# Kernel tuning notes

Measured on AMD Instinct MI355X. Metric: run time of the kernel, lower is better.

## Reference

```python
import jax, jax.numpy as jnp
import numpy as np

N = 50000
E = 800000
IN_C = 128
MSG_C = 64
OUT_C = 128


def setup_inputs() -> dict:
    key = jax.random.key(0)
    ks = jax.random.split(key, 10)
    x = jax.random.normal(ks[0], (N, IN_C), dtype=jnp.float32)
    edge_index = jax.random.randint(ks[1], (2, E), 0, N, dtype=jnp.int64)
    message = jax.random.normal(ks[2], (E, MSG_C), dtype=jnp.float32)
    # MLP params (Linear stores [out,in] in torch; we keep [in,out] for x @ W)
    s1 = 1.0 / np.sqrt(IN_C + MSG_C)
    s2 = 1.0 / np.sqrt(OUT_C)
    W1 = jax.random.uniform(ks[3], (IN_C + MSG_C, OUT_C), minval=-s1, maxval=s1, dtype=jnp.float32)
    b1 = jax.random.uniform(ks[4], (OUT_C,), minval=-s1, maxval=s1, dtype=jnp.float32)
    W2 = jax.random.uniform(ks[5], (OUT_C, OUT_C), minval=-s2, maxval=s2, dtype=jnp.float32)
    b2 = jax.random.uniform(ks[6], (OUT_C,), minval=-s2, maxval=s2, dtype=jnp.float32)
    W3 = jax.random.uniform(ks[7], (OUT_C, OUT_C), minval=-s2, maxval=s2, dtype=jnp.float32)
    gamma = jnp.ones((OUT_C,), dtype=jnp.float32)
    beta = jnp.zeros((OUT_C,), dtype=jnp.float32)
    return {"x": x, "edge_index": edge_index, "message": message,
            "W1": W1, "b1": b1, "W2": W2, "b2": b2, "W3": W3,
            "gamma": gamma, "beta": beta}


def _layer_norm(h, gamma, beta, eps=1e-5):
    mu = jnp.mean(h, axis=-1, keepdims=True)
    var = jnp.mean((h - mu) ** 2, axis=-1, keepdims=True)
    return (h - mu) * jax.lax.rsqrt(var + eps) * gamma + beta


def reference(x, edge_index, message, W1, b1, W2, b2, W3, gamma, beta):
    dest = edge_index[1]
    # scatter-add messages into N node slots: [E, msg] -> [N, msg]
    msg_aggr = jax.ops.segment_sum(message, dest, num_segments=N)
    h = jnp.concatenate([x, msg_aggr], axis=-1)  # [N, in+msg]
    h = jax.nn.leaky_relu(h @ W1 + b1, negative_slope=0.2)
    h = jax.nn.leaky_relu(h @ W2 + b2, negative_slope=0.2)
    h = h @ W3  # no bias
    return _layer_norm(h, gamma, beta)
```

## Files before the change

kernel.cpp:

```cpp
#include <hip/hip_runtime.h>

#define N_NODES 50000
#define N_EDGES 800000
#define IN_C 128
#define MSG_C 64
#define OUT_C 128
#define SCAN_NB 49

typedef __attribute__((ext_vector_type(8))) short short8v;
typedef __attribute__((ext_vector_type(4))) float f32x4;
typedef __attribute__((ext_vector_type(2))) unsigned int u32x2;
typedef __attribute__((ext_vector_type(4))) unsigned int u32x4;

__device__ __forceinline__ unsigned short f2bf(float f) {
    union { float f; unsigned int u; } v; v.f = f;
    unsigned int r = (v.u + 0x7FFFu + ((v.u >> 16) & 1u)) >> 16;
    return (unsigned short)r;
}
__device__ __forceinline__ float bflo(unsigned u) {
    union { unsigned u; float f; } v; v.u = u << 16; return v.f;
}
__device__ __forceinline__ float bfhi(unsigned u) {
    union { unsigned u; float f; } v; v.u = u & 0xFFFF0000u; return v.f;
}

__global__ __launch_bounds__(256) void init_kernel(
    int4* __restrict__ deg4,
    const float* __restrict__ W1, const float* __restrict__ W2,
    const float* __restrict__ W3, unsigned short* __restrict__ Wt1,
    unsigned short* __restrict__ Wt2, unsigned short* __restrict__ Wt3)
{
    int idx = blockIdx.x * 256 + threadIdx.x;
    if (idx < 12500) deg4[idx] = make_int4(0, 0, 0, 0);
    if (idx < 24576) {
        int k = idx >> 7, n = idx & 127;
        Wt1[n * 192 + k] = f2bf(W1[idx]);
    } else if (idx < 40960) {
        int t = idx - 24576;
        int k = t >> 7, n = t & 127;
        Wt2[n * 128 + k] = f2bf(W2[t]);
    } else if (idx < 57344) {
        int t = idx - 40960;
        int k = t >> 7, n = t & 127;
        Wt3[n * 128 + k] = f2bf(W3[t]);
    }
}

__global__ __launch_bounds__(256) void hist_kernel(const int* __restrict__ edge_index,
                                                   int* __restrict__ deg)
{
    int i = blockIdx.x * 256 + threadIdx.x;
    if (i >= N_EDGES / 4) return;
    int4 d4 = *reinterpret_cast<const int4*>(edge_index + N_EDGES + i * 4);
    atomicAdd(&deg[d4.x], 1);
    atomicAdd(&deg[d4.y], 1);
    atomicAdd(&deg[d4.z], 1);
    atomicAdd(&deg[d4.w], 1);
}

__global__ __launch_bounds__(1024) void scan_a_kernel(const int* __restrict__ deg,
                                                      int* __restrict__ offsets,
                                                      int* __restrict__ bsum)
{
    __shared__ int wsum[16];
    const int tid = threadIdx.x, lane = tid & 63, wid = tid >> 6;
    int i = blockIdx.x * 1024 + tid;
    int v = (i < N_NODES) ? deg[i] : 0;
    int s = v;
    #pragma unroll
    for (int d = 1; d < 64; d <<= 1) {
        int t = __shfl_up(s, d);
        if (lane >= d) s += t;
    }
    if (lane == 63) wsum[wid] = s;
    __syncthreads();
    if (wid == 0 && lane < 16) {
        int ws = wsum[lane];
        int ss = ws;
        #pragma unroll
        for (int d = 1; d < 16; d <<= 1) {
            int t = __shfl_up(ss, d);
            if (lane >= d) ss += t;
        }
        wsum[lane] = ss - ws;
    }
    __syncthreads();
    if (i < N_NODES) offsets[i] = s - v + wsum[wid];
    if (tid == 1023) bsum[blockIdx.x] = wsum[15] + s;
}

__global__ __launch_bounds__(1024) void scan_bc_kernel(int* __restrict__ offsets,
                                                       int* __restrict__ cursor,
                                                       const int* __restrict__ bsum)
{
    __shared__ int bpre_s, btot_s;
    const int tid = threadIdx.x;
    if (tid < 64) {
        int v = (tid < SCAN_NB) ? bsum[tid] : 0;
        int s = v;
        #pragma unroll
        for (int d = 1; d < 64; d <<= 1) {
            int t = __shfl_up(s, d);
            if (tid >= d) s += t;
        }
        if (tid == (int)blockIdx.x) bpre_s = s - v;
        if (tid == SCAN_NB - 1) btot_s = s;
    }
    __syncthreads();
    int i = blockIdx.x * 1024 + tid;
    if (i < N_NODES) {
        int o = offsets[i] + bpre_s;
        offsets[i] = o;
        cursor[i] = o;
    }
    if (blockIdx.x == 0 && tid == 0) offsets[N_NODES] = btot_s;
}

__global__ __launch_bounds__(256) void permute_kernel(
    const int* __restrict__ edge_index, const float* __restrict__ message,
    int* __restrict__ cursor, unsigned int* __restrict__ pbuf)
{
    int t = blockIdx.x * 256 + threadIdx.x;
    int e = t >> 4;
    if (e >= N_EDGES) return;
    int lane = threadIdx.x & 63;
    int s = lane & 15;
    int dest = edge_index[N_EDGES + e];
    int pos = 0;
    if (s == 0) pos = atomicAdd(&cursor[dest], 1);
    pos = __shfl(pos, lane & 48);
    f32x4 v = __builtin_nontemporal_load(
        reinterpret_cast<const f32x4*>(message + (long)e * MSG_C + s * 4));
    u32x2 p;
    p.x = (unsigned)f2bf(v.x) | ((unsigned)f2bf(v.y) << 16);
    p.y = (unsigned)f2bf(v.z) | ((unsigned)f2bf(v.w) << 16);
    __builtin_nontemporal_store(p,
        reinterpret_cast<u32x2*>(pbuf + (long)pos * 32 + s * 2));
}

__global__ __launch_bounds__(256) void segsum_kernel(const int* __restrict__ offsets,
                                                     const u32x4* __restrict__ pbuf4,
                                                     unsigned int* __restrict__ aggr_u32)
{
    const int wid = threadIdx.x >> 6;
    const int lane = threadIdx.x & 63;
    int n = blockIdx.x * 4 + wid;
    if (n >= N_NODES) return;
    int s0 = offsets[n], e0 = offsets[n + 1];
    long base = (long)s0 * 8;
    int cnt = (e0 - s0) * 8;
    float a0 = 0.f, a1 = 0.f, a2 = 0.f, a3 = 0.f,
          a4 = 0.f, a5 = 0.f, a6 = 0.f, a7 = 0.f;
    for (int k = lane; k < cnt; k += 64) {
        u32x4 u = __builtin_nontemporal_load(pbuf4 + base + k);
        a0 += bflo(u.x); a1 += bfhi(u.x);
        a2 += bflo(u.y); a3 += bfhi(u.y);
        a4 += bflo(u.z); a5 += bfhi(u.z);
        a6 += bflo(u.w); a7 += bfhi(u.w);
    }
    #pragma unroll
    for (int m = 8; m <= 32; m <<= 1) {
        a0 += __shfl_xor(a0, m); a1 += __shfl_xor(a1, m);
        a2 += __shfl_xor(a2, m); a3 += __shfl_xor(a3, m);
        a4 += __shfl_xor(a4, m); a5 += __shfl_xor(a5, m);
        a6 += __shfl_xor(a6, m); a7 += __shfl_xor(a7, m);
    }
    if (lane < 8) {
        u32x4 p;
        p.x = (unsigned)f2bf(a0) | ((unsigned)f2bf(a1) << 16);
        p.y = (unsigned)f2bf(a2) | ((unsigned)f2bf(a3) << 16);
        p.z = (unsigned)f2bf(a4) | ((unsigned)f2bf(a5) << 16);
        p.w = (unsigned)f2bf(a6) | ((unsigned)f2bf(a7) << 16);
        *reinterpret_cast<u32x4*>(aggr_u32 + (long)n * 32 + lane * 4) = p;
    }
}

__device__ __forceinline__ void stage_load(const unsigned short* __restrict__ Wt,
                                           int KW, int k0, int tid, u32x4 r[4])
{
    const u32x4* src = reinterpret_cast<const u32x4*>(
        Wt + (size_t)(tid >> 1) * KW + k0 + (tid & 1) * 32);
    r[0] = src[0]; r[1] = src[1]; r[2] = src[2]; r[3] = src[3];
}

__device__ __forceinline__ void stage_write(unsigned short* __restrict__ sw,
                                            int tid, const u32x4 r[4])
{
    u32x4* dst = reinterpret_cast<u32x4*>(sw + (tid >> 1) * 72 + (tid & 1) * 32);
    dst[0] = r[0]; dst[1] = r[1]; dst[2] = r[2]; dst[3] = r[3];
}

template<int KW, bool BIAS>
__device__ __forceinline__ void gemm_layer_lds(
    const unsigned short* __restrict__ Wt, const float* __restrict__ bias,
    unsigned short* __restrict__ sW,
    const short8v* af, int tid, int lr, int lg, f32x4 acc[8])
{
    constexpr int NCH = KW / 64;
    #pragma unroll
    for (int ct = 0; ct < 8; ++ct) {
        float bv = BIAS ? bias[ct * 16 + lr] : 0.f;
        acc[ct] = (f32x4){bv, bv, bv, bv};
    }
    u32x4 r[4];
    stage_load(Wt, KW, 0, tid, r);
    stage_write(sW, tid, r);
    __syncthreads();
    #pragma unroll
    for (int c = 0; c < NCH; ++c) {
        if (c + 1 < NCH) stage_load(Wt, KW, (c + 1) * 64, tid, r);
        const unsigned short* swc = sW + (c & 1) * (128 * 72);
        #pragma unroll
        for (int k2 = 0; k2 < 2; ++k2) {
            #pragma unroll
            for (int ct = 0; ct < 8; ++ct) {
                short8v b = *reinterpret_cast<const short8v*>(
                    swc + (ct * 16 + lr) * 72 + k2 * 32 + lg * 8);
                acc[ct] = __builtin_amdgcn_mfma_f32_16x16x32_bf16(
                    af[c * 2 + k2], b, acc[ct], 0, 0, 0);
            }
        }
        if (c + 1 < NCH) stage_write(sW + ((c + 1) & 1) * (128 * 72), tid, r);
        __syncthreads();
    }
}

__device__ __forceinline__ void store_h_leaky(unsigned short* __restrict__ H,
                                              int lr, int lg, const f32x4 acc[8])
{
    #pragma unroll
    for (int ct = 0; ct < 8; ++ct)
        #pragma unroll
        for (int j = 0; j < 4; ++j) {
            float v = acc[ct][j];
            v = v > 0.f ? v : 0.2f * v;
            H[(lg * 4 + j) * 136 + ct * 16 + lr] = f2bf(v);
        }
}

__global__ __launch_bounds__(256, 2) void mlp_mfma_kernel(
    const float* __restrict__ x, const unsigned short* __restrict__ aggr_bf,
    const unsigned short* __restrict__ Wt1, const float* __restrict__ b1,
    const unsigned short* __restrict__ Wt2, const float* __restrict__ b2,
    const unsigned short* __restrict__ Wt3, const float* __restrict__ gamma,
    const float* __restrict__ beta, float* __restrict__ out)
{
    __shared__ __align__(16) unsigned short sA0[4][16][200];
    __shared__ __align__(16) unsigned short sH[4][16][136];
    __shared__ __align__(16) unsigned short sW[2 * 128 * 72];

    const int tid = threadIdx.x;
    const int w = tid >> 6, l = tid & 63;
    const int lr = l & 15, lg = l >> 4;
    const int R0 = blockIdx.x * 64 + w * 16;
    const bool act = (R0 < N_NODES);

    #pragma unroll
    for (int i = 0; i < 4; ++i) {
        int r = lg + i * 4;
        int c0 = lr * 8;
        int gr = R0 + r;
        float4 v0 = {}, v1 = {};
        if (gr < N_NODES) {
            const float4* xp = reinterpret_cast<const float4*>(x + (size_t)gr * IN_C + c0);
            v0 = xp[0]; v1 = xp[1];
        }
        uint4 p;
        p.x = (unsigned)f2bf(v0.x) | ((unsigned)f2bf(v0.y) << 16);
        p.y = (unsigned)f2bf(v0.z) | ((unsigned)f2bf(v0.w) << 16);
        p.z = (unsigned)f2bf(v1.x) | ((unsigned)f2bf(v1.y) << 16);
        p.w = (unsigned)f2bf(v1.z) | ((unsigned)f2bf(v1.w) << 16);
        *reinterpret_cast<uint4*>(&sA0[w][r][c0]) = p;
    }
    #pragma unroll
    for (int i = 0; i < 2; ++i) {
        int r = (l >> 3) + i * 8;
        int c0 = (l & 7) * 8;
        int gr = R0 + r;
        uint4 a4 = {};
        if (gr < N_NODES)
            a4 = *reinterpret_cast<const uint4*>(aggr_bf + (size_t)gr * MSG_C + c0);
        *reinterpret_cast<uint4*>(&sA0[w][r][IN_C + c0]) = a4;
    }

    f32x4 acc[8];
    short8v af[6];

    #pragma unroll
    for (int ks = 0; ks < 6; ++ks)
        af[ks] = *reinterpret_cast<const short8v*>(&sA0[w][lr][ks * 32 + lg * 8]);
    gemm_layer_lds<192, true>(Wt1, b1, sW, af, tid, lr, lg, acc);
    store_h_leaky(&sH[w][0][0], lr, lg, acc);

    #pragma unroll
    for (int ks = 0; ks < 4; ++ks)
        af[ks] = *reinterpret_cast<const short8v*>(&sH[w][lr][ks * 32 + lg * 8]);
    gemm_layer_lds<128, true>(Wt2, b2, sW, af, tid, lr, lg, acc);
    store_h_leaky(&sH[w][0][0], lr, lg, acc);

    #pragma unroll
    for (int ks = 0; ks < 4; ++ks)
        af[ks] = *reinterpret_cast<const short8v*>(&sH[w][lr][ks * 32 + lg * 8]);
    gemm_layer_lds<128, false>(Wt3, nullptr, sW, af, tid, lr, lg, acc);

    float g8[8], be8[8];
    #pragma unroll
    for (int ct = 0; ct < 8; ++ct) {
        g8[ct] = gamma[ct * 16 + lr];
        be8[ct] = beta[ct * 16 + lr];
    }
    #pragma unroll
    for (int j = 0; j < 4; ++j) {
        float s1 = 0.f, s2 = 0.f;
        #pragma unroll
        for (int ct = 0; ct < 8; ++ct) {
            float v = acc[ct][j];
            s1 += v; s2 += v * v;
        }
        #pragma unroll
        for (int m = 8; m >= 1; m >>= 1) {
            s1 += __shfl_xor(s1, m);
            s2 += __shfl_xor(s2, m);
        }
        float mu = s1 * (1.f / 128.f);
        float var = s2 * (1.f / 128.f) - mu * mu;
        float rs = rsqrtf(var + 1e-5f);
        int gr = R0 + lg * 4 + j;
        if (act && gr < N_NODES) {
            #pragma unroll
            for (int ct = 0; ct < 8; ++ct)
                out[(size_t)gr * OUT_C + ct * 16 + lr] =
                    (acc[ct][j] - mu) * rs * g8[ct] + be8[ct];
        }
    }
}

extern "C" void kernel_launch(void* const* d_in, const int* in_sizes, int n_in,
                              void* d_out, int out_size, void* d_ws, size_t ws_size,
                              hipStream_t stream)
{
    const float* x       = (const float*)d_in[0];
    const int*   edge    = (const int*)d_in[1];
    const float* message = (const float*)d_in[2];
    const float* W1      = (const float*)d_in[3];
    const float* b1      = (const float*)d_in[4];
    const float* W2      = (const float*)d_in[5];
    const float* b2      = (const float*)d_in[6];
    const float* W3      = (const float*)d_in[7];
    const float* gamma   = (const float*)d_in[8];
    const float* beta    = (const float*)d_in[9];
    float* out  = (float*)d_out;

    char* ws = (char*)d_ws;
    unsigned short* aggr_bf = (unsigned short*)(ws);
    int*   deg     = (int*)(ws + 6400000);
    int*   cursor  = (int*)(ws + 6600000);
    int*   offsets = (int*)(ws + 6800000);
    int*   bsum    = (int*)(ws + 7000016);
    unsigned short* Wt1 = (unsigned short*)(ws + 7000224);
    unsigned short* Wt2 = (unsigned short*)(ws + 7049376);
    unsigned short* Wt3 = (unsigned short*)(ws + 7082144);
    unsigned int* pbuf  = (unsigned int*)(ws + 7115008);

    init_kernel<<<224, 256, 0, stream>>>((int4*)deg, W1, W2, W3, Wt1, Wt2, Wt3);

    int qblocks = (N_EDGES / 4 + 255) / 256;
    hist_kernel<<<qblocks, 256, 0, stream>>>(edge, deg);
    scan_a_kernel<<<SCAN_NB, 1024, 0, stream>>>(deg, offsets, bsum);
    scan_bc_kernel<<<SCAN_NB, 1024, 0, stream>>>(offsets, cursor, bsum);

    permute_kernel<<<N_EDGES * 16 / 256, 256, 0, stream>>>(edge, message, cursor, pbuf);

    segsum_kernel<<<(N_NODES + 3) / 4, 256, 0, stream>>>(
        offsets, (const u32x4*)pbuf, (unsigned int*)aggr_bf);

    mlp_mfma_kernel<<<(N_NODES + 63) / 64, 256, 0, stream>>>(
        x, aggr_bf, Wt1, b1, Wt2, b2, Wt3, gamma, beta, out);
}
```

Before: 165.5 us.

## Fuse segment-sum aggregation into MLP kernel prologue

Removes the separate segsum kernel. Each wavefront in the MLP kernel now reduces the permuted bf16 messages for its 16 rows and writes the sums straight into shared memory. This drops one launch and the write and re-read of the aggregated buffer in global memory. The cost is that the reduction loop runs serially per row within a wave, with less parallelism and latency hiding than the standalone kernel, which could stall the MFMA stage.

```diff
diff --git a/kernel.cpp b/kernel.cpp
--- a/kernel.cpp
+++ b/kernel.cpp
@@ -138,43 +138,6 @@
         reinterpret_cast<u32x2*>(pbuf + (long)pos * 32 + s * 2));
 }
 
-__global__ __launch_bounds__(256) void segsum_kernel(const int* __restrict__ offsets,
-                                                     const u32x4* __restrict__ pbuf4,
-                                                     unsigned int* __restrict__ aggr_u32)
-{
-    const int wid = threadIdx.x >> 6;
-    const int lane = threadIdx.x & 63;
-    int n = blockIdx.x * 4 + wid;
-    if (n >= N_NODES) return;
-    int s0 = offsets[n], e0 = offsets[n + 1];
-    long base = (long)s0 * 8;
-    int cnt = (e0 - s0) * 8;
-    float a0 = 0.f, a1 = 0.f, a2 = 0.f, a3 = 0.f,
-          a4 = 0.f, a5 = 0.f, a6 = 0.f, a7 = 0.f;
-    for (int k = lane; k < cnt; k += 64) {
-        u32x4 u = __builtin_nontemporal_load(pbuf4 + base + k);
-        a0 += bflo(u.x); a1 += bfhi(u.x);
-        a2 += bflo(u.y); a3 += bfhi(u.y);
-        a4 += bflo(u.z); a5 += bfhi(u.z);
-        a6 += bflo(u.w); a7 += bfhi(u.w);
-    }
-    #pragma unroll
-    for (int m = 8; m <= 32; m <<= 1) {
-        a0 += __shfl_xor(a0, m); a1 += __shfl_xor(a1, m);
-        a2 += __shfl_xor(a2, m); a3 += __shfl_xor(a3, m);
-        a4 += __shfl_xor(a4, m); a5 += __shfl_xor(a5, m);
-        a6 += __shfl_xor(a6, m); a7 += __shfl_xor(a7, m);
-    }
-    if (lane < 8) {
-        u32x4 p;
-        p.x = (unsigned)f2bf(a0) | ((unsigned)f2bf(a1) << 16);
-        p.y = (unsigned)f2bf(a2) | ((unsigned)f2bf(a3) << 16);
-        p.z = (unsigned)f2bf(a4) | ((unsigned)f2bf(a5) << 16);
-        p.w = (unsigned)f2bf(a6) | ((unsigned)f2bf(a7) << 16);
-        *reinterpret_cast<u32x4*>(aggr_u32 + (long)n * 32 + lane * 4) = p;
-    }
-}
-
 __device__ __forceinline__ void stage_load(const unsigned short* __restrict__ Wt,
                                            int KW, int k0, int tid, u32x4 r[4])
 {
@@ -239,7 +202,8 @@
 }
 
 __global__ __launch_bounds__(256, 2) void mlp_mfma_kernel(
-    const float* __restrict__ x, const unsigned short* __restrict__ aggr_bf,
+    const float* __restrict__ x, const int* __restrict__ offsets,
+    const u32x4* __restrict__ pbuf4,
     const unsigned short* __restrict__ Wt1, const float* __restrict__ b1,
     const unsigned short* __restrict__ Wt2, const float* __restrict__ b2,
     const unsigned short* __restrict__ Wt3, const float* __restrict__ gamma,
@@ -272,15 +236,44 @@
         p.w = (unsigned)f2bf(v1.z) | ((unsigned)f2bf(v1.w) << 16);
         *reinterpret_cast<uint4*>(&sA0[w][r][c0]) = p;
     }
-    #pragma unroll
-    for (int i = 0; i < 2; ++i) {
-        int r = (l >> 3) + i * 8;
-        int c0 = (l & 7) * 8;
-        int gr = R0 + r;
-        uint4 a4 = {};
-        if (gr < N_NODES)
-            a4 = *reinterpret_cast<const uint4*>(aggr_bf + (size_t)gr * MSG_C + c0);
-        *reinterpret_cast<uint4*>(&sA0[w][r][IN_C + c0]) = a4;
+
+    if (act) {
+        #pragma unroll 1
+        for (int m = 0; m < 16; ++m) {
+            int n = R0 + m;
+            int s0 = offsets[n], e0 = offsets[n + 1];
+            long base = (long)s0 * 8;
+            int cntel = (e0 - s0) * 8;
+            float a0 = 0.f, a1 = 0.f, a2 = 0.f, a3 = 0.f,
+                  a4 = 0.f, a5 = 0.f, a6 = 0.f, a7 = 0.f;
+            for (int k = l; k < cntel; k += 64) {
+                u32x4 u = __builtin_nontemporal_load(pbuf4 + base + k);
+                a0 += bflo(u.x); a1 += bfhi(u.x);
+                a2 += bflo(u.y); a3 += bfhi(u.y);
+                a4 += bflo(u.z); a5 += bfhi(u.z);
+                a6 += bflo(u.w); a7 += bfhi(u.w);
+            }
+            #pragma unroll
+            for (int mm = 8; mm <= 32; mm <<= 1) {
+                a0 += __shfl_xor(a0, mm); a1 += __shfl_xor(a1, mm);
+                a2 += __shfl_xor(a2, mm); a3 += __shfl_xor(a3, mm);
+                a4 += __shfl_xor(a4, mm); a5 += __shfl_xor(a5, mm);
+                a6 += __shfl_xor(a6, mm); a7 += __shfl_xor(a7, mm);
+            }
+            if (l < 8) {
+                uint4 p;
+                p.x = (unsigned)f2bf(a0) | ((unsigned)f2bf(a1) << 16);
+                p.y = (unsigned)f2bf(a2) | ((unsigned)f2bf(a3) << 16);
+                p.z = (unsigned)f2bf(a4) | ((unsigned)f2bf(a5) << 16);
+                p.w = (unsigned)f2bf(a6) | ((unsigned)f2bf(a7) << 16);
+                *reinterpret_cast<uint4*>(&sA0[w][m][IN_C + l * 8]) = p;
+            }
+        }
+    } else if (l < 8) {
+        uint4 z = {};
+        #pragma unroll
+        for (int m = 0; m < 16; ++m)
+            *reinterpret_cast<uint4*>(&sA0[w][m][IN_C + l * 8]) = z;
     }
 
     f32x4 acc[8];
@@ -352,15 +345,14 @@
     float* out  = (float*)d_out;
 
     char* ws = (char*)d_ws;
-    unsigned short* aggr_bf = (unsigned short*)(ws);
-    int*   deg     = (int*)(ws + 6400000);
-    int*   cursor  = (int*)(ws + 6600000);
-    int*   offsets = (int*)(ws + 6800000);
-    int*   bsum    = (int*)(ws + 7000016);
-    unsigned short* Wt1 = (unsigned short*)(ws + 7000224);
-    unsigned short* Wt2 = (unsigned short*)(ws + 7049376);
-    unsigned short* Wt3 = (unsigned short*)(ws + 7082144);
-    unsigned int* pbuf  = (unsigned int*)(ws + 7115008);
+    int*   deg     = (int*)(ws);
+    int*   cursor  = (int*)(ws + 200000);
+    int*   offsets = (int*)(ws + 400000);
+    int*   bsum    = (int*)(ws + 600016);
+    unsigned short* Wt1 = (unsigned short*)(ws + 600224);
+    unsigned short* Wt2 = (unsigned short*)(ws + 649376);
+    unsigned short* Wt3 = (unsigned short*)(ws + 682144);
+    unsigned int* pbuf  = (unsigned int*)(ws + 714912);
 
     init_kernel<<<224, 256, 0, stream>>>((int4*)deg, W1, W2, W3, Wt1, Wt2, Wt3);
 
@@ -371,9 +363,6 @@
 
     permute_kernel<<<N_EDGES * 16 / 256, 256, 0, stream>>>(edge, message, cursor, pbuf);
 
-    segsum_kernel<<<(N_NODES + 3) / 4, 256, 0, stream>>>(
-        offsets, (const u32x4*)pbuf, (unsigned int*)aggr_bf);
-
     mlp_mfma_kernel<<<(N_NODES + 63) / 64, 256, 0, stream>>>(
-        x, aggr_bf, Wt1, b1, Wt2, b2, Wt3, gamma, beta, out);
-}
+        x, offsets, (const u32x4*)pbuf, Wt1, b1, Wt2, b2, Wt3, gamma, beta, out);
+}
```

Result: slower. 266.1 us (+60.8%).
